# Kernel tuning notes

Hardware: AMD Instinct MI355X
Metric: run time of the kernel (lower is better)

## Reference

```python
import jax, jax.numpy as jnp
import numpy as np

HIDDEN = 3584
H = 28          # num attention heads
KV = 4          # num key-value heads
HD = 128        # head dim
MROPE = [16, 24, 24]  # sum*2 == HD
EPS = 1e-6
S_TOT = 4096
N_SAMPLES = 4


def rmsnorm(x, w, eps=EPS):
    return x * jax.lax.rsqrt(jnp.mean(x * x, axis=-1, keepdims=True) + eps) * w


def rotate_half(x):
    x1, x2 = jnp.split(x, 2, axis=-1)
    return jnp.concatenate([-x2, x1], axis=-1)


def mrope_merge(t):
    # t: [3, S, HD] -> [S, HD], section i taken from rope axis i%3
    cuts = np.cumsum(np.array(MROPE) * 2)[:-1]
    parts = jnp.split(t, cuts, axis=-1)
    return jnp.concatenate([p[i % 3] for i, p in enumerate(parts)], axis=-1)


def setup_inputs() -> dict:
    key = jax.random.key(0)
    ks = iter(jax.random.split(key, 32))
    std = 0.02

    def w(shape):
        return jax.random.normal(next(ks), shape, dtype=jnp.float32) * std

    inp = {
        "packed_sequence": jax.random.normal(next(ks), (S_TOT, HIDDEN), dtype=jnp.float32),
        "packed_cos": jax.random.uniform(next(ks), (3, S_TOT, HD), dtype=jnp.float32, minval=-1.0, maxval=1.0),
        "packed_sin": jax.random.uniform(next(ks), (3, S_TOT, HD), dtype=jnp.float32, minval=-1.0, maxval=1.0),
    }
    # und / geo indices partition [0, S_TOT)
    inp["packed_und_token_indexes"] = jnp.arange(S_TOT // 2, dtype=jnp.int64 if jax.config.jax_enable_x64 else jnp.int32)
    inp["packed_geo_token_indexes"] = jnp.arange(S_TOT // 2, dtype=inp["packed_und_token_indexes"].dtype) + S_TOT // 2
    inp["sample_len"] = S_TOT // N_SAMPLES

    for tag in ("und", "geo"):
        inp[f"q_w_{tag}"] = w((H * HD, HIDDEN))
        inp[f"q_b_{tag}"] = jnp.zeros((H * HD,), jnp.float32)
        inp[f"k_w_{tag}"] = w((KV * HD, HIDDEN))
        inp[f"k_b_{tag}"] = jnp.zeros((KV * HD,), jnp.float32)
        inp[f"v_w_{tag}"] = w((KV * HD, HIDDEN))
        inp[f"v_b_{tag}"] = jnp.zeros((KV * HD,), jnp.float32)
        inp[f"o_w_{tag}"] = w((HIDDEN, H * HD))
        inp[f"q_norm_{tag}"] = jnp.ones((HD,), jnp.float32)
        inp[f"k_norm_{tag}"] = jnp.ones((HD,), jnp.float32)
    return inp


def reference(packed_sequence, packed_cos, packed_sin,
              q_w_und, q_b_und, k_w_und, k_b_und, v_w_und, v_b_und, o_w_und,
              q_norm_und, k_norm_und,
              q_w_geo, q_b_geo, k_w_geo, k_b_geo, v_w_geo, v_b_geo, o_w_geo,
              q_norm_geo, k_norm_geo,
              packed_und_token_indexes, packed_geo_token_indexes, sample_len):
    S, D = packed_sequence.shape
    G = H // KV
    und, geo = packed_und_token_indexes, packed_geo_token_indexes
    xu = packed_sequence[und]
    xg = packed_sequence[geo]

    def scatter(dim, fu, fg):
        out = jnp.zeros((S, dim), packed_sequence.dtype)
        return out.at[und].set(fu).at[geo].set(fg)

    # modality-routed QKV projections (gather -> gemm -> scatter)
    q = scatter(H * HD, xu @ q_w_und.T + q_b_und, xg @ q_w_geo.T + q_b_geo).reshape(S, H, HD)
    k = scatter(KV * HD, xu @ k_w_und.T + k_b_und, xg @ k_w_geo.T + k_b_geo).reshape(S, KV, HD)
    v = scatter(KV * HD, xu @ v_w_und.T + v_b_und, xg @ v_w_geo.T + v_b_geo).reshape(S, KV, HD)

    # per-modality QK RMSNorm
    qn = jnp.zeros_like(q).at[und].set(rmsnorm(q[und], q_norm_und)).at[geo].set(rmsnorm(q[geo], q_norm_geo))
    kn = jnp.zeros_like(k).at[und].set(rmsnorm(k[und], k_norm_und)).at[geo].set(rmsnorm(k[geo], k_norm_geo))

    # multimodal rotary embedding
    cos = mrope_merge(packed_cos)[:, None, :]  # [S,1,HD]
    sin = mrope_merge(packed_sin)[:, None, :]
    qr = qn * cos + rotate_half(qn) * sin
    kr = kn * cos + rotate_half(kn) * sin

    # block-diagonal causal attention over packed equal-length samples
    L = int(sample_len)
    B = S // L
    qb = qr.reshape(B, L, H, HD)
    kb = jnp.repeat(kr.reshape(B, L, KV, HD), G, axis=2)  # GQA expansion
    vb = jnp.repeat(v.reshape(B, L, KV, HD), G, axis=2)
    scores = jnp.einsum('blhd,bmhd->bhlm', qb, kb) / np.sqrt(HD).astype(np.float32)
    causal = jnp.tril(jnp.ones((L, L), bool))
    scores = jnp.where(causal, scores, jnp.finfo(scores.dtype).min)
    attn = jax.nn.softmax(scores, axis=-1)
    out = jnp.einsum('bhlm,bmhd->blhd', attn, vb).reshape(S, H * HD)

    # modality-routed output projection
    res = jnp.zeros((S, D), packed_sequence.dtype)
    res = res.at[und].set(out[und] @ o_w_und.T).at[geo].set(out[geo] @ o_w_geo.T)
    return res
```

## Files before the change

kernel.cpp:

```cpp
#include <hip/hip_runtime.h>
#include <hip/hip_bf16.h>
#include <stdint.h>

#define HIDDEN 3584
#define NH 28
#define NKV 4
#define HD 128
#define GQ (NH / NKV)
#define NQKV ((NH + 2 * NKV) * HD)
#define LSAMP 1024

typedef __bf16 bf16x8 __attribute__((ext_vector_type(8)));
typedef float f32x4 __attribute__((ext_vector_type(4)));

__device__ __forceinline__ unsigned short f2bf(float f) {
  unsigned int u = __float_as_uint(f);
  u += 0x7fffu + ((u >> 16) & 1u);
  return (unsigned short)(u >> 16);
}
__device__ __forceinline__ float bf2f(unsigned short h) {
  return __uint_as_float(((unsigned int)h) << 16);
}

__device__ __forceinline__ void gload16(const void* g, void* l) {
  __builtin_amdgcn_global_load_lds(
      (const __attribute__((address_space(1))) void*)g,
      (__attribute__((address_space(3))) void*)l, 16, 0, 0);
}

__global__ void build_maps_kernel(const int* __restrict__ und, const int* __restrict__ geo,
                                  int nu, int ng,
                                  int* __restrict__ row_of_token, int* __restrict__ tok_of_row,
                                  int* __restrict__ mod_of_token) {
  int i = blockIdx.x * 256 + threadIdx.x;
  if (i < nu) {
    int t = und[i];
    row_of_token[t] = i; tok_of_row[i] = t; mod_of_token[t] = 0;
  } else if (i < nu + ng) {
    int j = i - nu;
    int t = geo[j];
    row_of_token[t] = nu + j; tok_of_row[nu + j] = t; mod_of_token[t] = 1;
  }
}

struct Cvt8 {
  const float* src[8];
  unsigned short* dst[8];
  int cum[8];
};
__global__ void convert_gather_kernel(Cvt8 a, int cvt4,
                                      const float* __restrict__ X,
                                      const int* __restrict__ tok_of_row,
                                      unsigned short* __restrict__ Xg, int tot4) {
  int i = blockIdx.x * blockDim.x + threadIdx.x;
  const int stride = gridDim.x * blockDim.x;
  for (; i < tot4; i += stride) {
    if (i < cvt4) {
      int seg = 0;
#pragma unroll
      for (int s2 = 1; s2 < 8; ++s2) seg += (i >= a.cum[s2]);
      const int off = i - a.cum[seg];
      float4 v = reinterpret_cast<const float4*>(a.src[seg])[off];
      reinterpret_cast<ushort4*>(a.dst[seg])[off] =
          make_ushort4(f2bf(v.x), f2bf(v.y), f2bf(v.z), f2bf(v.w));
    } else {
      const int gi = i - cvt4;
      const int r = gi / (HIDDEN / 4);
      const int c = gi - r * (HIDDEN / 4);
      const int tok = tok_of_row[r];
      float4 v = reinterpret_cast<const float4*>(X + (size_t)tok * HIDDEN)[c];
      reinterpret_cast<ushort4*>(Xg)[(size_t)r * (HIDDEN / 4) + c] =
          make_ushort4(f2bf(v.x), f2bf(v.y), f2bf(v.z), f2bf(v.w));
    }
  }
}

template <int OUTMODE, int NT, int WR, int WC, int NF>
__global__ __launch_bounds__(NT, (NT / 64 + 3) / 4)
void gemm2_kernel(const unsigned short* __restrict__ A,
                  const unsigned short* __restrict__ W0, const unsigned short* __restrict__ W1,
                  const float* __restrict__ qb0, const float* __restrict__ kb0, const float* __restrict__ vb0,
                  const float* __restrict__ qb1, const float* __restrict__ kb1, const float* __restrict__ vb1,
                  unsigned short* __restrict__ Obf, float* __restrict__ Of32,
                  const int* __restrict__ tok_of_row,
                  int nu, int ng, int N, int K, int NX, int NY) {
  constexpr int MF = 256 / WR / 16;
  constexpr int BN = WC * NF * 16;
  constexpr int BUFSZ = 32768 + BN * 128;
  constexpr int ACH = 2048;
  constexpr int BCH = BN * 8;
  __shared__ char lds[2 * BUFSZ];

  const int nwg = NX * NY * 2;
  int id = blockIdx.x + NX * (blockIdx.y + NY * blockIdx.z);
  {
    const int q = nwg >> 3, r = nwg & 7;
    const int xcd = id & 7, pos = id >> 3;
    id = (xcd < r ? xcd * (q + 1) : r * (q + 1) + (xcd - r) * q) + pos;
  }
  const int bx = id % NX;
  const int byz = id / NX;
  const int by = byz % NY;
  const int bz = byz / NY;

  const int baseRow = bz ? nu : 0;
  const int Mcount = bz ? ng : nu;
  const int mbase = by * 256;
  if (mbase >= Mcount) return;
  const unsigned short* W = bz ? W1 : W0;

  const int t = threadIdx.x;
  const int w = t >> 6, l = t & 63;
  const int l15 = l & 15, l4 = l >> 4;
  const int wr = w / WC, wc = w % WC;
  const int wrr = wr * (MF * 16), wcc = wc * (NF * 16);
  const int ncol0 = bx * BN;
  const int krev = w & 1;

  f32x4 acc[MF][NF] = {};

  const int nk = K >> 6;

  auto stage = [&](int bufIdx, int kt) {
    char* base = lds + bufIdx * BUFSZ;
    const int k0 = kt * 64;
#pragma unroll
    for (int c0 = 0; c0 < ACH; c0 += NT) {
      const int c = c0 + t;
      if (c < ACH) {
        const int row = c >> 3, slot = c & 7;
        const int srck = (slot ^ (row & 7)) << 3;
        int ar = mbase + row; if (ar >= Mcount) ar = Mcount - 1;
        gload16(A + (size_t)(baseRow + ar) * K + k0 + srck, base + c * 16);
      }
    }
#pragma unroll
    for (int c0 = 0; c0 < BCH; c0 += NT) {
      const int c = c0 + t;
      if (c < BCH) {
        const int row = c >> 3, slot = c & 7;
        const int srck = (slot ^ (row & 7)) << 3;
        gload16(W + (size_t)(ncol0 + row) * K + k0 + srck, base + 32768 + c * 16);
      }
    }
  };

  stage(0, 0);
  asm volatile("s_waitcnt vmcnt(0)\n\ts_barrier" ::: "memory");

  for (int kt = 0; kt < nk; ++kt) {
    char* Ab = lds + (kt & 1) * BUFSZ;
    char* Bb = Ab + 32768;

    if (kt + 1 < nk) stage((kt + 1) & 1, kt + 1);
    __builtin_amdgcn_sched_barrier(0);

#pragma unroll
    for (int ks = 0; ks < 2; ++ks) {
      const int kss = krev ? (1 - ks) : ks;
      bf16x8 af[MF], bfr[NF];
#pragma unroll
      for (int mf = 0; mf < MF; ++mf) {
        const int row = wrr + mf * 16 + l15;
        af[mf] = *reinterpret_cast<const bf16x8*>(Ab + row * 128 + (((kss * 4 + l4) ^ (row & 7)) << 4));
      }
#pragma unroll
      for (int nf = 0; nf < NF; ++nf) {
        const int row = wcc + nf * 16 + l15;
        bfr[nf] = *reinterpret_cast<const bf16x8*>(Bb + row * 128 + (((kss * 4 + l4) ^ (row & 7)) << 4));
      }
      __builtin_amdgcn_s_setprio(1);
#pragma unroll
      for (int mf = 0; mf < MF; ++mf)
#pragma unroll
        for (int nf = 0; nf < NF; ++nf)
          acc[mf][nf] = __builtin_amdgcn_mfma_f32_16x16x32_bf16(af[mf], bfr[nf], acc[mf][nf], 0, 0, 0);
      __builtin_amdgcn_s_setprio(0);
    }

    if (kt + 1 < nk) {
      asm volatile("s_waitcnt vmcnt(0)\n\ts_barrier" ::: "memory");
    }
  }

#pragma unroll
  for (int mf = 0; mf < MF; ++mf) {
#pragma unroll
    for (int rr = 0; rr < 4; ++rr) {
      const int ml = mbase + wrr + mf * 16 + l4 * 4 + rr;
      if (ml >= Mcount) continue;
      int trow = 0;
      if (OUTMODE == 1) trow = tok_of_row[baseRow + ml];
#pragma unroll
      for (int nf = 0; nf < NF; ++nf) {
        const int n = ncol0 + wcc + nf * 16 + l15;
        const float v = acc[mf][nf][rr];
        if (OUTMODE == 0) {
          const float* qb = bz ? qb1 : qb0;
          const float* kb = bz ? kb1 : kb0;
          const float* vb = bz ? vb1 : vb0;
          const float bias = (n < NH * HD) ? qb[n]
                              : ((n < (NH + NKV) * HD) ? kb[n - NH * HD] : vb[n - (NH + NKV) * HD]);
          Obf[(size_t)(baseRow + ml) * N + n] = f2bf(v + bias);
        } else {
          Of32[(size_t)trow * N + n] = v;
        }
      }
    }
  }
}

__global__ __launch_bounds__(64)
void norm_rope_kernel(const unsigned short* __restrict__ Y,
                      const int* __restrict__ row_of_token, const int* __restrict__ mod_of_token,
                      const float* __restrict__ pcos, const float* __restrict__ psin,
                      const float* __restrict__ qn_u, const float* __restrict__ kn_u,
                      const float* __restrict__ qn_g, const float* __restrict__ kn_g,
                      unsigned short* __restrict__ Qr,
                      unsigned short* __restrict__ Kr,
                      unsigned short* __restrict__ Vt,
                      int S) {
  const int s = blockIdx.x, l = threadIdx.x;
  const int g = l >> 4, l15 = l & 15;
  const int d0 = l15 * 8;
  const int axis = (d0 < 32) ? 0 : (d0 < 80 ? 1 : 2);
  const int r = row_of_token[s];
  const int m = mod_of_token[s];
  const float* qn = m ? qn_g : qn_u;
  const float* kn = m ? kn_g : kn_u;
  const bool hi = l15 >= 8;
  const float rsign = hi ? 1.f : -1.f;
  constexpr float SC = 0.08838834764831845f;

  float c8[8], s8[8], qw8[8], kw8[8];
  {
    const float* cp = pcos + ((size_t)axis * S + s) * HD + d0;
    const float* sp = psin + ((size_t)axis * S + s) * HD + d0;
#pragma unroll
    for (int j = 0; j < 8; ++j) { c8[j] = cp[j]; s8[j] = sp[j]; }
#pragma unroll
    for (int j = 0; j < 8; ++j) { qw8[j] = qn[d0 + j]; kw8[j] = kn[d0 + j]; }
  }
  const unsigned short* yrow = Y + (size_t)r * NQKV;

#pragma unroll
  for (int grp = 0; grp < 7; ++grp) {
    const int hh = grp * 4 + g;
    const bf16x8 y = *reinterpret_cast<const bf16x8*>(yrow + hh * HD + d0);
    float x[8], xw[8];
    float ss = 0.f;
#pragma unroll
    for (int j = 0; j < 8; ++j) { x[j] = bf2f(((unsigned short*)&y)[j]); ss += x[j] * x[j]; }
#pragma unroll
    for (int dd = 1; dd < 16; dd <<= 1) ss += __shfl_xor(ss, dd);
    const float rs = rsqrtf(ss * (1.f / 128.f) + 1e-6f) * SC;
#pragma unroll
    for (int j = 0; j < 8; ++j) xw[j] = x[j] * qw8[j];
    unsigned short o[8];
#pragma unroll
    for (int j = 0; j < 8; ++j) {
      const float xp = __shfl_xor(xw[j], 8);
      o[j] = f2bf(rs * (xw[j] * c8[j] + rsign * xp * s8[j]));
    }
    *reinterpret_cast<ushort4*>(Qr + ((size_t)hh * S + s) * HD + d0) = make_ushort4(o[0], o[1], o[2], o[3]);
    *reinterpret_cast<ushort4*>(Qr + ((size_t)hh * S + s) * HD + d0 + 4) = make_ushort4(o[4], o[5], o[6], o[7]);
  }

  {
    const int kh = g;
    const bf16x8 y = *reinterpret_cast<const bf16x8*>(yrow + (NH + kh) * HD + d0);
    float x[8], xw[8];
    float ss = 0.f;
#pragma unroll
    for (int j = 0; j < 8; ++j) { x[j] = bf2f(((unsigned short*)&y)[j]); ss += x[j] * x[j]; }
#pragma unroll
    for (int dd = 1; dd < 16; dd <<= 1) ss += __shfl_xor(ss, dd);
    const float rs = rsqrtf(ss * (1.f / 128.f) + 1e-6f);
#pragma unroll
    for (int j = 0; j < 8; ++j) xw[j] = x[j] * kw8[j];
    unsigned short o[8];
#pragma unroll
    for (int j = 0; j < 8; ++j) {
      const float xp = __shfl_xor(xw[j], 8);
      o[j] = f2bf(rs * (xw[j] * c8[j] + rsign * xp * s8[j]));
    }
    *reinterpret_cast<ushort4*>(Kr + ((size_t)kh * S + s) * HD + d0) = make_ushort4(o[0], o[1], o[2], o[3]);
    *reinterpret_cast<ushort4*>(Kr + ((size_t)kh * S + s) * HD + d0 + 4) = make_ushort4(o[4], o[5], o[6], o[7]);
  }

  {
    const int vh = g;
    const bf16x8 y = *reinterpret_cast<const bf16x8*>(yrow + (NH + NKV + vh) * HD + d0);
#pragma unroll
    for (int j = 0; j < 8; ++j)
      Vt[((size_t)(vh * HD + d0 + j)) * S + s] = ((unsigned short*)&y)[j];
  }
}

__global__ __launch_bounds__(448, 1)
void attn7_kernel(const unsigned short* __restrict__ Qr, const unsigned short* __restrict__ Kr,
                  const unsigned short* __restrict__ Vt, const int* __restrict__ row_of_token,
                  unsigned short* __restrict__ Og, int S) {
  __shared__ char lds[2 * 16384 + 2 * 16384 + 7 * 4608];
  const int kvh = blockIdx.y, b = blockIdx.z;
  const int t = threadIdx.x, w = t >> 6, l = t & 63;
  const int l15 = l & 15, l4 = l >> 4;
  const int h = kvh * GQ + w;
  const int sbase = b * LSAMP;
  char* Plds = lds + 65536 + w * 4608;

  auto stage = [&](int bufIdx, int kt) {
    char* Kb = lds + bufIdx * 16384;
    char* Vb = lds + 32768 + bufIdx * 16384;
    const int kb0 = sbase + kt * 64;
    for (int c = t; c < 1024; c += 448) {
      const int row = c >> 4, slot = c & 15;
      const int srcs = slot ^ (row & 15);
      gload16(Kr + ((size_t)kvh * S + kb0 + row) * HD + srcs * 8, Kb + c * 16);
    }
    for (int c = t; c < 1024; c += 448) {
      const int row = c >> 3, slot = c & 7;
      const int srcs = slot ^ (row & 7);
      gload16(Vt + (size_t)(kvh * HD + row) * S + kb0 + srcs * 8, Vb + c * 16);
    }
  };

  for (int pass = 0; pass < 2; ++pass) {
    const int q32 = pass ? (31 - blockIdx.x) : blockIdx.x;
    const int nkt = q32 / 2 + 1;

    bf16x8 aq[2][4];
#pragma unroll
    for (int fr = 0; fr < 2; ++fr) {
      const int qrow = sbase + q32 * 32 + fr * 16 + l15;
      const unsigned short* qp = Qr + ((size_t)h * S + qrow) * HD + l4 * 8;
#pragma unroll
      for (int kk = 0; kk < 4; ++kk) aq[fr][kk] = *reinterpret_cast<const bf16x8*>(qp + kk * 32);
    }
    f32x4 acc[2][8] = {};
    float mr[2][4], lr[2][4];
#pragma unroll
    for (int fr = 0; fr < 2; ++fr)
#pragma unroll
      for (int rr = 0; rr < 4; ++rr) { mr[fr][rr] = -INFINITY; lr[fr][rr] = 0.f; }

    stage(0, 0);
    asm volatile("s_waitcnt vmcnt(0)\n\ts_barrier" ::: "memory");

    for (int kt = 0; kt < nkt; ++kt) {
      char* Kb = lds + (kt & 1) * 16384;
      char* Vb = lds + 32768 + (kt & 1) * 16384;

      if (kt + 1 < nkt) stage((kt + 1) & 1, kt + 1);
      __builtin_amdgcn_sched_barrier(0);

      f32x4 sa[2][4] = {};
#pragma unroll
      for (int kk = 0; kk < 4; ++kk) {
        bf16x8 bk[4];
#pragma unroll
        for (int nf = 0; nf < 4; ++nf) {
          const int row = nf * 16 + l15;
          const int slot = kk * 4 + l4;
          bk[nf] = *reinterpret_cast<const bf16x8*>(Kb + row * 256 + ((slot ^ (row & 15)) << 4));
        }
#pragma unroll
        for (int fr = 0; fr < 2; ++fr)
#pragma unroll
          for (int nf = 0; nf < 4; ++nf)
            sa[fr][nf] = __builtin_amdgcn_mfma_f32_16x16x32_bf16(aq[fr][kk], bk[nf], sa[fr][nf], 0, 0, 0);
      }

#pragma unroll
      for (int fr = 0; fr < 2; ++fr) {
        const int qg = q32 * 32 + fr * 16 + l4 * 4;
#pragma unroll
        for (int nf = 0; nf < 4; ++nf) {
          const int cg = kt * 64 + nf * 16 + l15;
#pragma unroll
          for (int rr = 0; rr < 4; ++rr)
            if (cg > qg + rr) sa[fr][nf][rr] = -INFINITY;
        }
#pragma unroll
        for (int rr = 0; rr < 4; ++rr) {
          float mx = fmaxf(fmaxf(sa[fr][0][rr], sa[fr][1][rr]), fmaxf(sa[fr][2][rr], sa[fr][3][rr]));
          mx = fmaxf(mx, mr[fr][rr]);
#pragma unroll
          for (int dd = 1; dd < 16; dd <<= 1) mx = fmaxf(mx, __shfl_xor(mx, dd));
          const float alpha = __expf(mr[fr][rr] - mx);
          mr[fr][rr] = mx;
          float part = 0.f;
#pragma unroll
          for (int nf = 0; nf < 4; ++nf) {
            const float p = __expf(sa[fr][nf][rr] - mx);
            sa[fr][nf][rr] = p;
            part += p;
          }
          lr[fr][rr] = lr[fr][rr] * alpha + part;
#pragma unroll
          for (int nf2 = 0; nf2 < 8; ++nf2) acc[fr][nf2][rr] *= alpha;
        }
#pragma unroll
        for (int rr = 0; rr < 4; ++rr) {
          const int row = fr * 16 + l4 * 4 + rr;
#pragma unroll
          for (int nf = 0; nf < 4; ++nf)
            ((unsigned short*)(Plds + row * 144))[nf * 16 + l15] = f2bf(sa[fr][nf][rr]);
        }
      }

#pragma unroll
      for (int kk2 = 0; kk2 < 2; ++kk2) {
        bf16x8 ap[2];
#pragma unroll
        for (int fr = 0; fr < 2; ++fr)
          ap[fr] = *reinterpret_cast<const bf16x8*>(Plds + (fr * 16 + l15) * 144 + kk2 * 64 + l4 * 16);
#pragma unroll
        for (int nf2 = 0; nf2 < 8; ++nf2) {
          const int rowd = nf2 * 16 + l15;
          const int slot = kk2 * 4 + l4;
          const bf16x8 bv = *reinterpret_cast<const bf16x8*>(Vb + rowd * 128 + ((slot ^ (rowd & 7)) << 4));
#pragma unroll
          for (int fr = 0; fr < 2; ++fr)
            acc[fr][nf2] = __builtin_amdgcn_mfma_f32_16x16x32_bf16(ap[fr], bv, acc[fr][nf2], 0, 0, 0);
        }
      }

      if (kt + 1 < nkt) {
        asm volatile("s_waitcnt vmcnt(0)\n\ts_barrier" ::: "memory");
      }
    }

#pragma unroll
    for (int fr = 0; fr < 2; ++fr) {
#pragma unroll
      for (int rr = 0; rr < 4; ++rr) {
#pragma unroll
        for (int dd = 1; dd < 16; dd <<= 1) lr[fr][rr] += __shfl_xor(lr[fr][rr], dd);
        const float inv = 1.f / lr[fr][rr];
        const int srow = sbase + q32 * 32 + fr * 16 + l4 * 4 + rr;
        const int mrow = row_of_token[srow];
        unsigned short* orow = Og + (size_t)mrow * (NH * HD) + h * HD;
#pragma unroll
        for (int nf2 = 0; nf2 < 8; ++nf2) orow[nf2 * 16 + l15] = f2bf(acc[fr][nf2][rr] * inv);
      }
    }

    if (pass == 0) {
      asm volatile("s_waitcnt vmcnt(0) lgkmcnt(0)\n\ts_barrier" ::: "memory");
    }
  }
}

extern "C" void kernel_launch(void* const* d_in, const int* in_sizes, int n_in,
                              void* d_out, int out_size, void* d_ws, size_t ws_size,
                              hipStream_t stream) {
  const float* X = (const float*)d_in[0];
  const float* pcos = (const float*)d_in[1];
  const float* psin = (const float*)d_in[2];
  const int* und = (const int*)d_in[3];
  const int* geo = (const int*)d_in[4];
  const int nu = in_sizes[3], ng = in_sizes[4];
  const int S = in_sizes[0] / HIDDEN;

  const float* qw[2] = {(const float*)d_in[6], (const float*)d_in[15]};
  const float* qb[2] = {(const float*)d_in[7], (const float*)d_in[16]};
  const float* kw[2] = {(const float*)d_in[8], (const float*)d_in[17]};
  const float* kb[2] = {(const float*)d_in[9], (const float*)d_in[18]};
  const float* vw[2] = {(const float*)d_in[10], (const float*)d_in[19]};
  const float* vb[2] = {(const float*)d_in[11], (const float*)d_in[20]};
  const float* ow[2] = {(const float*)d_in[12], (const float*)d_in[21]};
  const float* qn[2] = {(const float*)d_in[13], (const float*)d_in[22]};
  const float* kn[2] = {(const float*)d_in[14], (const float*)d_in[23]};

  char* ws = (char*)d_ws;
  size_t off = 0;
  auto alloc = [&](size_t bytes) {
    char* p = ws + off;
    off = (off + bytes + 255) & ~(size_t)255;
    return p;
  };
  int* row_of_token = (int*)alloc((size_t)S * 4);
  int* tok_of_row = (int*)alloc((size_t)S * 4);
  int* mod_of_token = (int*)alloc((size_t)S * 4);
  unsigned short* Wqkv[2] = {(unsigned short*)alloc((size_t)NQKV * HIDDEN * 2),
                             (unsigned short*)alloc((size_t)NQKV * HIDDEN * 2)};
  unsigned short* Wo[2] = {(unsigned short*)alloc((size_t)HIDDEN * HIDDEN * 2),
                           (unsigned short*)alloc((size_t)HIDDEN * HIDDEN * 2)};
  unsigned short* Xg = (unsigned short*)alloc((size_t)S * HIDDEN * 2);
  unsigned short* Yqkv = (unsigned short*)alloc((size_t)S * NQKV * 2);
  unsigned short* Qr = (unsigned short*)alloc((size_t)NH * S * HD * 2);
  unsigned short* Kr = (unsigned short*)alloc((size_t)NKV * S * HD * 2);
  unsigned short* Vt = (unsigned short*)alloc((size_t)NKV * S * HD * 2);
  unsigned short* Og = (unsigned short*)alloc((size_t)S * NH * HD * 2);
  (void)ws_size; (void)n_in; (void)out_size;

  build_maps_kernel<<<(S + 255) / 256, 256, 0, stream>>>(und, geo, nu, ng,
                                                         row_of_token, tok_of_row, mod_of_token);
  {
    Cvt8 ca;
    const float* srcs[8] = {qw[0], kw[0], vw[0], ow[0], qw[1], kw[1], vw[1], ow[1]};
    unsigned short* dsts[8] = {
        Wqkv[0], Wqkv[0] + (size_t)NH * HD * HIDDEN, Wqkv[0] + (size_t)(NH + NKV) * HD * HIDDEN, Wo[0],
        Wqkv[1], Wqkv[1] + (size_t)NH * HD * HIDDEN, Wqkv[1] + (size_t)(NH + NKV) * HD * HIDDEN, Wo[1]};
    const int n4s[8] = {NH * HD * HIDDEN / 4, NKV * HD * HIDDEN / 4, NKV * HD * HIDDEN / 4, HIDDEN * HIDDEN / 4,
                        NH * HD * HIDDEN / 4, NKV * HD * HIDDEN / 4, NKV * HD * HIDDEN / 4, HIDDEN * HIDDEN / 4};
    int cum = 0;
    for (int i = 0; i < 8; ++i) { ca.src[i] = srcs[i]; ca.dst[i] = dsts[i]; ca.cum[i] = cum; cum += n4s[i]; }
    const int gather4 = S * (HIDDEN / 4);
    convert_gather_kernel<<<2048, 256, 0, stream>>>(ca, cum, X, tok_of_row, Xg, cum + gather4);
  }

  const int maxM = (nu > ng ? nu : ng);
  {
    const int NX = NQKV / 288, NY = (maxM + 255) / 256;
    gemm2_kernel<0, 768, 4, 3, 6><<<dim3(NX, NY, 2), 768, 0, stream>>>(
        Xg, Wqkv[0], Wqkv[1], qb[0], kb[0], vb[0], qb[1], kb[1], vb[1],
        Yqkv, nullptr, nullptr, nu, ng, NQKV, HIDDEN, NX, NY);
  }

  norm_rope_kernel<<<S, 64, 0, stream>>>(Yqkv, row_of_token, mod_of_token, pcos, psin,
                                         qn[0], kn[0], qn[1], kn[1], Qr, Kr, Vt, S);

  attn7_kernel<<<dim3(16, NKV, S / LSAMP), 448, 0, stream>>>(Qr, Kr, Vt, row_of_token, Og, S);

  {
    const int NX = HIDDEN / 224, NY = (maxM + 255) / 256;
    gemm2_kernel<1, 512, 4, 2, 7><<<dim3(NX, NY, 2), 512, 0, stream>>>(
        Og, Wo[0], Wo[1], nullptr, nullptr, nullptr, nullptr, nullptr, nullptr,
        nullptr, (float*)d_out, tok_of_row, nu, ng, HIDDEN, HIDDEN, NX, NY);
  }
}
```

Measured before the change: 390.2 us.

## Add 256x256-tile output-projection GEMM with XCD-aware remap and phased MFMA

Replaces the generic gemm2 for the output projection with a dedicated kernel that uses 256x256 tiles (NX=14 instead of 16 tiles of 224 columns). It double-buffers A/B in 128KB of LDS with XOR-swizzled layout, interleaves the next-tile global loads between four MFMA phases with barriers and setprio, and remaps workgroup ids so neighbouring tiles land on the same XCD. The aim is better data reuse per tile and overlap of loads with compute. The cost is fewer workgroups (14x8x2 = 224 on the device), which may underfill the CUs, and 128KB of LDS per block, which limits occupancy.

```diff
diff --git a/kernel.cpp b/kernel.cpp
--- a/kernel.cpp
+++ b/kernel.cpp
@@ -205,6 +205,170 @@
         } else {
           Of32[(size_t)trow * N + n] = v;
         }
+      }
+    }
+  }
+}
+
+__global__ __launch_bounds__(512, 2)
+void gemm256o_kernel(const unsigned short* __restrict__ A,
+                     const unsigned short* __restrict__ W0, const unsigned short* __restrict__ W1,
+                     float* __restrict__ Of32, const int* __restrict__ tok_of_row,
+                     int nu, int ng, int N, int K, int NX, int NY) {
+  __shared__ char lds[131072];
+  const int nwg = NX * NY * 2;
+  int id = blockIdx.x + NX * (blockIdx.y + NY * blockIdx.z);
+  {
+    const int q = nwg >> 3, r = nwg & 7;
+    const int xcd = id & 7, pos = id >> 3;
+    id = (xcd < r ? xcd * (q + 1) : r * (q + 1) + (xcd - r) * q) + pos;
+  }
+  const int bx = id % NX;
+  const int byz = id / NX;
+  const int by = byz % NY;
+  const int bz = byz / NY;
+
+  const int baseRow = bz ? nu : 0;
+  const int Mcount = bz ? ng : nu;
+  const int mbase = by * 256;
+  if (mbase >= Mcount) return;
+  const unsigned short* W = bz ? W1 : W0;
+
+  const int t = threadIdx.x;
+  const int w = t >> 6, l = t & 63;
+  const int l15 = l & 15, l4 = l >> 4;
+  const int wr = w >> 2, wc = w & 3;
+  const int wrr = wr * 128, wcc = wc * 64;
+  const int ncol0 = bx * 256;
+
+  f32x4 acc[8][4] = {};
+  const int nk = K >> 6;
+
+  auto stageA = [&](int bufIdx, int kt) {
+    char* base = lds + bufIdx * 65536;
+    const int k0 = kt * 64;
+#pragma unroll
+    for (int i = 0; i < 4; ++i) {
+      const int c = t + i * 512;
+      const int row = c >> 3, slot = c & 7;
+      const int srck = (slot ^ (row & 7)) << 3;
+      int ar = mbase + row; if (ar >= Mcount) ar = Mcount - 1;
+      gload16(A + (size_t)(baseRow + ar) * K + k0 + srck, base + c * 16);
+    }
+  };
+  auto stageB = [&](int bufIdx, int kt) {
+    char* base = lds + bufIdx * 65536 + 32768;
+    const int k0 = kt * 64;
+#pragma unroll
+    for (int i = 0; i < 4; ++i) {
+      const int c = t + i * 512;
+      const int row = c >> 3, slot = c & 7;
+      const int srck = (slot ^ (row & 7)) << 3;
+      gload16(W + (size_t)(ncol0 + row) * K + k0 + srck, base + c * 16);
+    }
+  };
+
+  stageA(0, 0); stageB(0, 0);
+  asm volatile("s_waitcnt vmcnt(0)\n\ts_barrier" ::: "memory");
+
+  for (int kt = 0; kt < nk; ++kt) {
+    char* Ab = lds + (kt & 1) * 65536;
+    char* Bb = Ab + 32768;
+    const bool pre = (kt + 1 < nk);
+    const int nb = (kt + 1) & 1;
+    bf16x8 af[4], bfr[4];
+
+#pragma unroll
+    for (int mf = 0; mf < 4; ++mf) {
+      const int row = wrr + mf * 16 + l15;
+      af[mf] = *reinterpret_cast<const bf16x8*>(Ab + row * 128 + ((l4 ^ (row & 7)) << 4));
+    }
+#pragma unroll
+    for (int nf = 0; nf < 4; ++nf) {
+      const int row = wcc + nf * 16 + l15;
+      bfr[nf] = *reinterpret_cast<const bf16x8*>(Bb + row * 128 + ((l4 ^ (row & 7)) << 4));
+    }
+    if (pre) stageA(nb, kt + 1);
+    asm volatile("s_barrier" ::: "memory");
+    __builtin_amdgcn_sched_barrier(0);
+    __builtin_amdgcn_s_setprio(1);
+#pragma unroll
+    for (int mf = 0; mf < 4; ++mf)
+#pragma unroll
+      for (int nf = 0; nf < 4; ++nf)
+        acc[mf][nf] = __builtin_amdgcn_mfma_f32_16x16x32_bf16(af[mf], bfr[nf], acc[mf][nf], 0, 0, 0);
+    __builtin_amdgcn_s_setprio(0);
+    asm volatile("s_barrier" ::: "memory");
+
+#pragma unroll
+    for (int mf = 0; mf < 4; ++mf) {
+      const int row = wrr + 64 + mf * 16 + l15;
+      af[mf] = *reinterpret_cast<const bf16x8*>(Ab + row * 128 + ((l4 ^ (row & 7)) << 4));
+    }
+    if (pre) stageB(nb, kt + 1);
+    asm volatile("s_barrier" ::: "memory");
+    __builtin_amdgcn_sched_barrier(0);
+    __builtin_amdgcn_s_setprio(1);
+#pragma unroll
+    for (int mf = 0; mf < 4; ++mf)
+#pragma unroll
+      for (int nf = 0; nf < 4; ++nf)
+        acc[4 + mf][nf] = __builtin_amdgcn_mfma_f32_16x16x32_bf16(af[mf], bfr[nf], acc[4 + mf][nf], 0, 0, 0);
+    __builtin_amdgcn_s_setprio(0);
+    asm volatile("s_barrier" ::: "memory");
+
+#pragma unroll
+    for (int mf = 0; mf < 4; ++mf) {
+      const int row = wrr + mf * 16 + l15;
+      af[mf] = *reinterpret_cast<const bf16x8*>(Ab + row * 128 + (((4 + l4) ^ (row & 7)) << 4));
+    }
+#pragma unroll
+    for (int nf = 0; nf < 4; ++nf) {
+      const int row = wcc + nf * 16 + l15;
+      bfr[nf] = *reinterpret_cast<const bf16x8*>(Bb + row * 128 + (((4 + l4) ^ (row & 7)) << 4));
+    }
+    asm volatile("s_barrier" ::: "memory");
+    __builtin_amdgcn_sched_barrier(0);
+    __builtin_amdgcn_s_setprio(1);
+#pragma unroll
+    for (int mf = 0; mf < 4; ++mf)
+#pragma unroll
+      for (int nf = 0; nf < 4; ++nf)
+        acc[mf][nf] = __builtin_amdgcn_mfma_f32_16x16x32_bf16(af[mf], bfr[nf], acc[mf][nf], 0, 0, 0);
+    __builtin_amdgcn_s_setprio(0);
+    asm volatile("s_barrier" ::: "memory");
+
+#pragma unroll
+    for (int mf = 0; mf < 4; ++mf) {
+      const int row = wrr + 64 + mf * 16 + l15;
+      af[mf] = *reinterpret_cast<const bf16x8*>(Ab + row * 128 + (((4 + l4) ^ (row & 7)) << 4));
+    }
+    asm volatile("s_barrier" ::: "memory");
+    __builtin_amdgcn_sched_barrier(0);
+    __builtin_amdgcn_s_setprio(1);
+#pragma unroll
+    for (int mf = 0; mf < 4; ++mf)
+#pragma unroll
+      for (int nf = 0; nf < 4; ++nf)
+        acc[4 + mf][nf] = __builtin_amdgcn_mfma_f32_16x16x32_bf16(af[mf], bfr[nf], acc[4 + mf][nf], 0, 0, 0);
+    __builtin_amdgcn_s_setprio(0);
+
+    if (pre) {
+      asm volatile("s_waitcnt vmcnt(0)\n\ts_barrier" ::: "memory");
+    }
+  }
+
+#pragma unroll
+  for (int mf = 0; mf < 8; ++mf) {
+#pragma unroll
+    for (int rr = 0; rr < 4; ++rr) {
+      const int ml = mbase + wrr + mf * 16 + l4 * 4 + rr;
+      if (ml >= Mcount) continue;
+      const int trow = tok_of_row[baseRow + ml];
+#pragma unroll
+      for (int nf = 0; nf < 4; ++nf) {
+        const int n = ncol0 + wcc + nf * 16 + l15;
+        Of32[(size_t)trow * N + n] = acc[mf][nf][rr];
       }
     }
   }
@@ -525,9 +689,8 @@
   attn7_kernel<<<dim3(16, NKV, S / LSAMP), 448, 0, stream>>>(Qr, Kr, Vt, row_of_token, Og, S);
 
   {
-    const int NX = HIDDEN / 224, NY = (maxM + 255) / 256;
-    gemm2_kernel<1, 512, 4, 2, 7><<<dim3(NX, NY, 2), 512, 0, stream>>>(
-        Og, Wo[0], Wo[1], nullptr, nullptr, nullptr, nullptr, nullptr, nullptr,
-        nullptr, (float*)d_out, tok_of_row, nu, ng, HIDDEN, HIDDEN, NX, NY);
-  }
-}
+    const int NX = HIDDEN / 256, NY = (maxM + 255) / 256;
+    gemm256o_kernel<<<dim3(NX, NY, 2), 512, 0, stream>>>(
+        Og, Wo[0], Wo[1], (float*)d_out, tok_of_row, nu, ng, HIDDEN, HIDDEN, NX, NY);
+  }
+}
```

After: 402.4 us. 3.1% more time.
